# Kernel tuning notes

Measured on AMD Instinct MI355X. Metric: run time of the kernel, lower is better.

Reference implementation:

```python
import jax, jax.numpy as jnp
import numpy as np

D_MODEL = 512
N_HEADS = 8
B, S = 2, 2048


def setup_inputs() -> dict:
    key = jax.random.key(0)
    ks = jax.random.split(key, 7)
    scale = 1.0 / np.sqrt(D_MODEL)
    return {
        "q": jax.random.normal(ks[0], (B, S, D_MODEL), jnp.float32),
        "k": jax.random.normal(ks[1], (B, S, D_MODEL), jnp.float32),
        "v": jax.random.normal(ks[2], (B, S, D_MODEL), jnp.float32),
        "Wq_w": jax.random.normal(ks[3], (D_MODEL, D_MODEL), jnp.float32) * scale,
        "Wq_b": jnp.zeros((D_MODEL,), jnp.float32),
        "Wc_w": jax.random.normal(ks[4], (D_MODEL, D_MODEL), jnp.float32) * scale,
        "Wc_b": jnp.zeros((D_MODEL,), jnp.float32),
    }


def _split(x, n_heads):
    b, s, d = x.shape
    return x.reshape(b, s, n_heads, d // n_heads).transpose(0, 2, 1, 3)  # [b,h,s,dh]


def reference(q, k, v, Wq_w, Wq_b, Wc_w, Wc_b):
    # NOTE: original code (faithfully) projects q, k, v all with W_q.
    qp = q @ Wq_w.T + Wq_b
    kp = k @ Wq_w.T + Wq_b
    vp = v @ Wq_w.T + Wq_b
    qh = _split(qp, N_HEADS)  # [b,h,s,dh]
    kh = _split(kp, N_HEADS)
    vh = _split(vp, N_HEADS)
    d_tensor = qh.shape[-1]
    scores = jnp.einsum("bhqd,bhkd->bhqk", qh, kh) / jnp.sqrt(jnp.float32(d_tensor))
    att = jax.nn.softmax(scores, axis=-1)
    out = jnp.einsum("bhqk,bhkd->bhqd", att, vh)
    b, h, s, dh = out.shape
    out = out.transpose(0, 2, 1, 3).reshape(b, s, h * dh)
    return out @ Wc_w.T + Wc_b
```

## Files before the change

### kernel.cpp

```cpp
#include <hip/hip_runtime.h>
#include <hip/hip_bf16.h>
#include <stdint.h>


typedef __bf16 bf16;
typedef __bf16 bvec8 __attribute__((ext_vector_type(8)));
typedef __bf16 bvec4 __attribute__((ext_vector_type(4)));
typedef float  fvec4 __attribute__((ext_vector_type(4)));
typedef float  fvec16 __attribute__((ext_vector_type(16)));
typedef int    ivec4 __attribute__((ext_vector_type(4)));

#define MFMA16(a, b, c) __builtin_amdgcn_mfma_f32_16x16x32_bf16(a, b, c, 0, 0, 0)
#define MFMA32(a, b, c) __builtin_amdgcn_mfma_f32_32x32x16_bf16(a, b, c, 0, 0, 0)

__device__ __forceinline__ void async16(const void* g, void* l) {
  __builtin_amdgcn_global_load_lds(
      (__attribute__((address_space(1))) void*)(g),
      (__attribute__((address_space(3))) void*)(l), 16, 0, 0);
}

__global__ void cvt_all(const float* __restrict__ q, const float* __restrict__ k,
                        const float* __restrict__ v, const float* __restrict__ Wq,
                        const float* __restrict__ Wc, bf16* __restrict__ qkvb,
                        bf16* __restrict__ Wq16, bf16* __restrict__ Wc16) {
  const int t = blockIdx.x * 256 + threadIdx.x;
  const float* src;
  bf16* dst;
  size_t i;
  if (t < 786432) {
    const int which = t >> 18;
    i = (size_t)(t & 262143);
    src = (which == 0) ? q : (which == 1) ? k : v;
    dst = qkvb + ((size_t)which << 21);
  } else if (t < 819200) {
    src = Wq; dst = Wq16; i = (size_t)(t - 786432);
  } else {
    src = Wc; dst = Wc16; i = (size_t)(t - 819200);
  }
  fvec4 a = *(const fvec4*)(src + i * 8);
  fvec4 b = *(const fvec4*)(src + i * 8 + 4);
  bvec8 o;
#pragma unroll
  for (int j = 0; j < 4; ++j) { o[j] = (bf16)a[j]; o[j + 4] = (bf16)b[j]; }
  *(bvec8*)(dst + i * 8) = o;
}

template <bool PROJ, typename OutT>
__launch_bounds__(256, 3)
__global__ void gemm512(const bf16* __restrict__ X, const bf16* __restrict__ W,
                        const float* __restrict__ bias, OutT* __restrict__ Y,
                        bf16* __restrict__ Yt) {
  __shared__ __attribute__((aligned(16))) char As[2][64 * 128];
  __shared__ __attribute__((aligned(16))) char Bs[2][128 * 128];

  const int tid = threadIdx.x;
  const int w = tid >> 6, l = tid & 63;
  const int wr = w >> 1, wc = w & 1;
  const int l15 = l & 15, lg = l >> 4;
  const int bm0 = blockIdx.x * 64;
  const int bn0 = blockIdx.y * 128;

  fvec4 acc[2][4] = {};

  auto stageA = [&](int buf, int k0) {
#pragma unroll
    for (int j = 0; j < 2; ++j) {
      int c = j * 256 + w * 64 + l;
      int row = c >> 3;
      int g = (c & 7) ^ (row & 7);
      async16(X + (size_t)(bm0 + row) * 512 + k0 + g * 8, &As[buf][c * 16]);
    }
  };
  auto stageB = [&](int buf, int k0) {
#pragma unroll
    for (int j = 0; j < 4; ++j) {
      int c = j * 256 + w * 64 + l;
      int row = c >> 3;
      int g = (c & 7) ^ (row & 7);
      async16(W + (size_t)(bn0 + row) * 512 + k0 + g * 8, &Bs[buf][c * 16]);
    }
  };

  stageA(0, 0);
  stageB(0, 0);
  __syncthreads();

  for (int t = 0; t < 8; ++t) {
    const int buf = t & 1;
    if (t < 7) { stageA(buf ^ 1, (t + 1) * 64); stageB(buf ^ 1, (t + 1) * 64); }
#pragma unroll
    for (int kk = 0; kk < 2; ++kk) {
      bvec8 af[2], bfr[4];
      const int g = kk * 4 + lg;
#pragma unroll
      for (int m = 0; m < 2; ++m) {
        int r = wr * 32 + m * 16 + l15;
        af[m] = *(const bvec8*)&As[buf][r * 128 + ((g ^ (r & 7)) << 4)];
      }
#pragma unroll
      for (int n = 0; n < 4; ++n) {
        int r = wc * 64 + n * 16 + l15;
        bfr[n] = *(const bvec8*)&Bs[buf][r * 128 + ((g ^ (r & 7)) << 4)];
      }
#pragma unroll
      for (int m = 0; m < 2; ++m)
#pragma unroll
        for (int n = 0; n < 4; ++n) acc[m][n] = MFMA16(af[m], bfr[n], acc[m][n]);
    }
    __syncthreads();
  }

  const bool trans = PROJ && (bm0 >= 8192);
#pragma unroll
  for (int n = 0; n < 4; ++n) {
    const int col = bn0 + wc * 64 + n * 16 + l15;
    const float bv = bias[col];
#pragma unroll
    for (int m = 0; m < 2; ++m) {
      const int row0 = bm0 + wr * 32 + m * 16 + lg * 4;
      if (!trans) {
#pragma unroll
        for (int r = 0; r < 4; ++r)
          Y[(size_t)(row0 + r) * 512 + col] = (OutT)(acc[m][n][r] + bv);
      } else {
        const int m0 = row0 - 8192;
        const int b = m0 >> 11, s = m0 & 2047;
        bvec4 v4;
#pragma unroll
        for (int r = 0; r < 4; ++r) v4[r] = (bf16)(acc[m][n][r] + bv);
        *(bvec4*)&Yt[(size_t)(b * 512 + col) * 2048 + s] = v4;
      }
    }
  }
}

__launch_bounds__(256, 3)
__global__ void attn_kernel(const bf16* __restrict__ qp, const bf16* __restrict__ kp,
                            const bf16* __restrict__ vt, bf16* __restrict__ po01,
                            bf16* __restrict__ po23, float* __restrict__ pl) {
  __shared__ __attribute__((aligned(16))) char Ks[2][64 * 128];
  __shared__ __attribute__((aligned(16))) char Vs[2][64 * 128];

  const int tid = threadIdx.x;
  const int w = tid >> 6, l = tid & 63;
  const int l31 = l & 31, hi = l >> 5;
  const int bh = blockIdx.y, b = bh >> 3, h = bh & 7;
  const int half = blockIdx.z;
  const int kvbase = half * 512;
  const int qw0 = blockIdx.x * 128 + w * 32;

  const bf16* kbase = kp + (size_t)(b * 2048) * 512 + h * 64;
  const bf16* vbase = vt + (size_t)(b * 512 + h * 64) * 2048;

  bvec8 qf[4];
  {
    const bf16* qrow = qp + (size_t)(b * 2048 + qw0 + l31) * 512 + h * 64 + hi * 8;
#pragma unroll
    for (int ks = 0; ks < 4; ++ks) qf[ks] = *(const bvec8*)(qrow + ks * 16);
  }

  auto stageK = [&](int buf, int kv0) {
#pragma unroll
    for (int j = 0; j < 2; ++j) {
      int c = j * 256 + tid;
      int row = c >> 3;
      int g = (c & 7) ^ (row & 7);
      async16(kbase + (size_t)(kv0 + row) * 512 + g * 8, &Ks[buf][c * 16]);
    }
  };
  auto stageV = [&](int buf, int kv0) {
#pragma unroll
    for (int j = 0; j < 2; ++j) {
      int c = j * 256 + tid;
      int row = c >> 3;
      int g = (c & 7) ^ (row & 7);
      async16(vbase + (size_t)row * 2048 + kv0 + g * 8, &Vs[buf][c * 16]);
    }
  };

  fvec16 oacc[2] = {};
  float l_run = 0.f;

  stageK(0, kvbase);
  stageV(0, kvbase);
  __syncthreads();

  const float SC = 0.125f * 1.44269504089f;

  for (int t = 0; t < 8; ++t) {
    const int buf = t & 1;
    if (t < 7) {
      stageK(buf ^ 1, kvbase + (t + 1) * 64);
      stageV(buf ^ 1, kvbase + (t + 1) * 64);
    }

    fvec16 sac[2] = {};
    __builtin_amdgcn_s_setprio(1);
#pragma unroll
    for (int ks = 0; ks < 4; ++ks) {
      const int chunk = ks * 2 + hi;
#pragma unroll
      for (int kvb = 0; kvb < 2; ++kvb) {
        const int r = kvb * 32 + l31;
        bvec8 kf = *(const bvec8*)&Ks[buf][r * 128 + ((chunk ^ (r & 7)) << 4)];
        sac[kvb] = MFMA32(kf, qf[ks], sac[kvb]);
      }
    }
    __builtin_amdgcn_s_setprio(0);

    ivec4 pw[4];
    float psum = 0.f;
#pragma unroll
    for (int f = 0; f < 2; ++f) {
      float p[16];
#pragma unroll
      for (int r2 = 0; r2 < 16; ++r2) {
        p[r2] = exp2f(sac[f][r2] * SC);
        psum += p[r2];
      }
      int wv[4][2];
#pragma unroll
      for (int m = 0; m < 4; ++m)
#pragma unroll
        for (int i = 0; i < 2; ++i)
          asm("v_cvt_pk_bf16_f32 %0, %1, %2"
              : "=v"(wv[m][i]) : "v"(p[4 * m + 2 * i]), "v"(p[4 * m + 2 * i + 1]));
#pragma unroll
      for (int i = 0; i < 2; ++i) {
        int a0 = wv[0][i], c0 = wv[1][i];
        asm volatile("v_permlane32_swap_b32 %0, %1" : "+v"(a0), "+v"(c0));
        pw[2 * f][i] = a0; pw[2 * f][2 + i] = c0;
        int a1 = wv[2][i], c1 = wv[3][i];
        asm volatile("v_permlane32_swap_b32 %0, %1" : "+v"(a1), "+v"(c1));
        pw[2 * f + 1][i] = a1; pw[2 * f + 1][2 + i] = c1;
      }
    }
    l_run += psum;

    __builtin_amdgcn_s_setprio(1);
#pragma unroll
    for (int ks = 0; ks < 4; ++ks) {
      const bvec8 pb = __builtin_bit_cast(bvec8, pw[ks]);
      const int chunk = ks * 2 + hi;
#pragma unroll
      for (int dhb = 0; dhb < 2; ++dhb) {
        const int r = dhb * 32 + l31;
        bvec8 vf = *(const bvec8*)&Vs[buf][r * 128 + ((chunk ^ (r & 7)) << 4)];
        oacc[dhb] = MFMA32(pb, vf, oacc[dhb]);
      }
    }
    __builtin_amdgcn_s_setprio(0);
    __syncthreads();
  }

  bf16* pob = ((half < 2) ? po01 : po23) + (size_t)(half & 1) * 2097152;
#pragma unroll
  for (int dhb = 0; dhb < 2; ++dhb)
#pragma unroll
    for (int r2 = 0; r2 < 16; ++r2) {
      const int q = qw0 + (r2 & 3) + 8 * (r2 >> 2) + 4 * hi;
      pob[(size_t)(b * 2048 + q) * 512 + h * 64 + dhb * 32 + l31] =
          (bf16)oacc[dhb][r2];
    }
  l_run += __shfl_xor(l_run, 32);
  if (hi == 0)
    pl[half * 32768 + (b * 2048 + qw0 + l31) * 8 + h] = l_run;
}

__global__ void combine_kernel(const bf16* __restrict__ po01, const bf16* __restrict__ po23,
                               const float* __restrict__ pl, bf16* __restrict__ att) {
  const int t = blockIdx.x * 256 + threadIdx.x;
  const int row = t >> 6;
  const int c8 = (t & 63) << 3;
  const int h = c8 >> 6;
  const float inv = 1.0f / (pl[row * 8 + h] + pl[32768 + row * 8 + h] +
                            pl[65536 + row * 8 + h] + pl[98304 + row * 8 + h]);
  bvec8 a0 = *(const bvec8*)(po01 + (size_t)row * 512 + c8);
  bvec8 a1 = *(const bvec8*)(po01 + 2097152 + (size_t)row * 512 + c8);
  bvec8 a2 = *(const bvec8*)(po23 + (size_t)row * 512 + c8);
  bvec8 a3 = *(const bvec8*)(po23 + 2097152 + (size_t)row * 512 + c8);
  bvec8 o;
#pragma unroll
  for (int j = 0; j < 8; ++j)
    o[j] = (bf16)((((float)a0[j] + (float)a1[j]) + ((float)a2[j] + (float)a3[j])) * inv);
  *(bvec8*)(att + (size_t)row * 512 + c8) = o;
}

extern "C" void kernel_launch(void* const* d_in, const int* in_sizes, int n_in,
                              void* d_out, int out_size, void* d_ws, size_t ws_size,
                              hipStream_t stream) {
  const float* q   = (const float*)d_in[0];
  const float* k   = (const float*)d_in[1];
  const float* v   = (const float*)d_in[2];
  const float* Wq  = (const float*)d_in[3];
  const float* Wqb = (const float*)d_in[4];
  const float* Wc  = (const float*)d_in[5];
  const float* Wcb = (const float*)d_in[6];
  float* out = (float*)d_out;

  char* ws = (char*)d_ws;
  const size_t MB = 1u << 20;
  bf16* qkvb = (bf16*)(ws);
  bf16* po01 = (bf16*)(ws);
  bf16* att  = (bf16*)(ws + 8 * MB);
  bf16* Wq16 = (bf16*)(ws + 12 * MB);
  bf16* Wc16 = (bf16*)(ws + 12 * MB + 512 * 1024);
  bf16* qkp  = (bf16*)(ws + 13 * MB);
  bf16* vt   = (bf16*)(ws + 21 * MB);
  bf16* po23 = (bf16*)(ws + 25 * MB);
  float* pl  = (float*)(ws + 33 * MB);

  dim3 bb(256);
  hipLaunchKernelGGL(cvt_all, dim3(3328), bb, 0, stream, q, k, v, Wq, Wc,
                     qkvb, Wq16, Wc16);
  hipLaunchKernelGGL((gemm512<true, bf16>), dim3(192, 4), bb, 0, stream,
                     qkvb, Wq16, Wqb, qkp, vt);
  hipLaunchKernelGGL(attn_kernel, dim3(16, 16, 4), bb, 0, stream,
                     qkp, qkp + 2097152, vt, po01, po23, pl);
  hipLaunchKernelGGL(combine_kernel, dim3(1024), bb, 0, stream, po01, po23, pl, att);
  hipLaunchKernelGGL((gemm512<false, float>), dim3(64, 4), bb, 0, stream,
                     att, Wc16, Wcb, out, nullptr);
}
```

Before: 69.97 us.

## Fuse fp32-to-bf16 conversion into GEMM loads and drop the convert kernel

```diff
diff --git a/kernel.cpp b/kernel.cpp
--- a/kernel.cpp
+++ b/kernel.cpp
@@ -19,37 +19,13 @@
       (__attribute__((address_space(3))) void*)(l), 16, 0, 0);
 }
 
-__global__ void cvt_all(const float* __restrict__ q, const float* __restrict__ k,
-                        const float* __restrict__ v, const float* __restrict__ Wq,
-                        const float* __restrict__ Wc, bf16* __restrict__ qkvb,
-                        bf16* __restrict__ Wq16, bf16* __restrict__ Wc16) {
-  const int t = blockIdx.x * 256 + threadIdx.x;
-  const float* src;
-  bf16* dst;
-  size_t i;
-  if (t < 786432) {
-    const int which = t >> 18;
-    i = (size_t)(t & 262143);
-    src = (which == 0) ? q : (which == 1) ? k : v;
-    dst = qkvb + ((size_t)which << 21);
-  } else if (t < 819200) {
-    src = Wq; dst = Wq16; i = (size_t)(t - 786432);
-  } else {
-    src = Wc; dst = Wc16; i = (size_t)(t - 819200);
-  }
-  fvec4 a = *(const fvec4*)(src + i * 8);
-  fvec4 b = *(const fvec4*)(src + i * 8 + 4);
-  bvec8 o;
-#pragma unroll
-  for (int j = 0; j < 4; ++j) { o[j] = (bf16)a[j]; o[j + 4] = (bf16)b[j]; }
-  *(bvec8*)(dst + i * 8) = o;
-}
-
 template <bool PROJ, typename OutT>
 __launch_bounds__(256, 3)
-__global__ void gemm512(const bf16* __restrict__ X, const bf16* __restrict__ W,
-                        const float* __restrict__ bias, OutT* __restrict__ Y,
-                        bf16* __restrict__ Yt) {
+__global__ void gemm_f32(const bf16* __restrict__ Abf,
+                         const float* __restrict__ Aq, const float* __restrict__ Ak,
+                         const float* __restrict__ Av, const float* __restrict__ Wf,
+                         const float* __restrict__ bias,
+                         OutT* __restrict__ Y, bf16* __restrict__ Yt) {
   __shared__ __attribute__((aligned(16))) char As[2][64 * 128];
   __shared__ __attribute__((aligned(16))) char Bs[2][128 * 128];
 
@@ -60,34 +36,82 @@
   const int bm0 = blockIdx.x * 64;
   const int bn0 = blockIdx.y * 128;
 
+  const float* Xs = nullptr;
+  int arow0 = 0;
+  if constexpr (PROJ) {
+    Xs = (bm0 < 4096) ? Aq : (bm0 < 8192) ? Ak : Av;
+    arow0 = bm0 & 4095;
+  }
+
   fvec4 acc[2][4] = {};
-
-  auto stageA = [&](int buf, int k0) {
+  fvec4 ra[2][2];
+  fvec4 rb[4][2];
+
+  auto loadA = [&](int k0) {
+    if constexpr (PROJ) {
+#pragma unroll
+      for (int j = 0; j < 2; ++j) {
+        int c = j * 256 + tid;
+        int row = c >> 3, g = (c & 7) ^ (row & 7);
+        const float* p = Xs + (size_t)(arow0 + row) * 512 + k0 + g * 8;
+        ra[j][0] = *(const fvec4*)p;
+        ra[j][1] = *(const fvec4*)(p + 4);
+      }
+    }
+  };
+  auto writeA = [&](int buf) {
+    if constexpr (PROJ) {
+#pragma unroll
+      for (int j = 0; j < 2; ++j) {
+        int c = j * 256 + tid;
+        bvec8 o;
+#pragma unroll
+        for (int e = 0; e < 4; ++e) { o[e] = (bf16)ra[j][0][e]; o[4 + e] = (bf16)ra[j][1][e]; }
+        *(bvec8*)&As[buf][c * 16] = o;
+      }
+    }
+  };
+  auto dmaA = [&](int buf, int k0) {
 #pragma unroll
     for (int j = 0; j < 2; ++j) {
-      int c = j * 256 + w * 64 + l;
-      int row = c >> 3;
-      int g = (c & 7) ^ (row & 7);
-      async16(X + (size_t)(bm0 + row) * 512 + k0 + g * 8, &As[buf][c * 16]);
-    }
-  };
-  auto stageB = [&](int buf, int k0) {
+      int c = j * 256 + tid;
+      int row = c >> 3, g = (c & 7) ^ (row & 7);
+      async16(Abf + (size_t)(bm0 + row) * 512 + k0 + g * 8, &As[buf][c * 16]);
+    }
+  };
+  auto loadB = [&](int k0) {
 #pragma unroll
     for (int j = 0; j < 4; ++j) {
-      int c = j * 256 + w * 64 + l;
-      int row = c >> 3;
-      int g = (c & 7) ^ (row & 7);
-      async16(W + (size_t)(bn0 + row) * 512 + k0 + g * 8, &Bs[buf][c * 16]);
-    }
-  };
-
-  stageA(0, 0);
-  stageB(0, 0);
+      int c = j * 256 + tid;
+      int row = c >> 3, g = (c & 7) ^ (row & 7);
+      const float* p = Wf + (size_t)(bn0 + row) * 512 + k0 + g * 8;
+      rb[j][0] = *(const fvec4*)p;
+      rb[j][1] = *(const fvec4*)(p + 4);
+    }
+  };
+  auto writeB = [&](int buf) {
+#pragma unroll
+    for (int j = 0; j < 4; ++j) {
+      int c = j * 256 + tid;
+      bvec8 o;
+#pragma unroll
+      for (int e = 0; e < 4; ++e) { o[e] = (bf16)rb[j][0][e]; o[4 + e] = (bf16)rb[j][1][e]; }
+      *(bvec8*)&Bs[buf][c * 16] = o;
+    }
+  };
+
+  if constexpr (PROJ) loadA(0); else dmaA(0, 0);
+  loadB(0);
+  writeA(0);
+  writeB(0);
   __syncthreads();
 
   for (int t = 0; t < 8; ++t) {
     const int buf = t & 1;
-    if (t < 7) { stageA(buf ^ 1, (t + 1) * 64); stageB(buf ^ 1, (t + 1) * 64); }
+    if (t < 7) {
+      if constexpr (PROJ) loadA((t + 1) * 64); else dmaA(buf ^ 1, (t + 1) * 64);
+      loadB((t + 1) * 64);
+    }
 #pragma unroll
     for (int kk = 0; kk < 2; ++kk) {
       bvec8 af[2], bfr[4];
@@ -106,6 +130,10 @@
       for (int m = 0; m < 2; ++m)
 #pragma unroll
         for (int n = 0; n < 4; ++n) acc[m][n] = MFMA16(af[m], bfr[n], acc[m][n]);
+    }
+    if (t < 7) {
+      writeA(buf ^ 1);
+      writeB(buf ^ 1);
     }
     __syncthreads();
   }
@@ -134,7 +162,7 @@
   }
 }
 
-__launch_bounds__(256, 3)
+__launch_bounds__(256, 4)
 __global__ void attn_kernel(const bf16* __restrict__ qp, const bf16* __restrict__ kp,
                             const bf16* __restrict__ vt, bf16* __restrict__ po01,
                             bf16* __restrict__ po23, float* __restrict__ pl) {
@@ -163,8 +191,7 @@
 #pragma unroll
     for (int j = 0; j < 2; ++j) {
       int c = j * 256 + tid;
-      int row = c >> 3;
-      int g = (c & 7) ^ (row & 7);
+      int row = c >> 3, g = (c & 7) ^ (row & 7);
       async16(kbase + (size_t)(kv0 + row) * 512 + g * 8, &Ks[buf][c * 16]);
     }
   };
@@ -172,8 +199,7 @@
 #pragma unroll
     for (int j = 0; j < 2; ++j) {
       int c = j * 256 + tid;
-      int row = c >> 3;
-      int g = (c & 7) ^ (row & 7);
+      int row = c >> 3, g = (c & 7) ^ (row & 7);
       async16(vbase + (size_t)row * 2048 + kv0 + g * 8, &Vs[buf][c * 16]);
     }
   };
@@ -300,24 +326,21 @@
 
   char* ws = (char*)d_ws;
   const size_t MB = 1u << 20;
-  bf16* qkvb = (bf16*)(ws);
   bf16* po01 = (bf16*)(ws);
   bf16* att  = (bf16*)(ws + 8 * MB);
-  bf16* Wq16 = (bf16*)(ws + 12 * MB);
-  bf16* Wc16 = (bf16*)(ws + 12 * MB + 512 * 1024);
   bf16* qkp  = (bf16*)(ws + 13 * MB);
   bf16* vt   = (bf16*)(ws + 21 * MB);
   bf16* po23 = (bf16*)(ws + 25 * MB);
   float* pl  = (float*)(ws + 33 * MB);
 
   dim3 bb(256);
-  hipLaunchKernelGGL(cvt_all, dim3(3328), bb, 0, stream, q, k, v, Wq, Wc,
-                     qkvb, Wq16, Wc16);
-  hipLaunchKernelGGL((gemm512<true, bf16>), dim3(192, 4), bb, 0, stream,
-                     qkvb, Wq16, Wqb, qkp, vt);
+  hipLaunchKernelGGL((gemm_f32<true, bf16>), dim3(192, 4), bb, 0, stream,
+                     (const bf16*)nullptr, q, k, v, Wq, Wqb, qkp, vt);
   hipLaunchKernelGGL(attn_kernel, dim3(16, 16, 4), bb, 0, stream,
                      qkp, qkp + 2097152, vt, po01, po23, pl);
-  hipLaunchKernelGGL(combine_kernel, dim3(1024), bb, 0, stream, po01, po23, pl, att);
-  hipLaunchKernelGGL((gemm512<false, float>), dim3(64, 4), bb, 0, stream,
-                     att, Wc16, Wcb, out, nullptr);
-}
+  hipLaunchKernelGGL(combine_kernel, dim3(1024), bb, 0, stream,
+                     po01, po23, pl, att);
+  hipLaunchKernelGGL((gemm_f32<false, float>), dim3(64, 4), bb, 0, stream,
+                     att, (const float*)nullptr, (const float*)nullptr,
+                     (const float*)nullptr, Wc, Wcb, out, (bf16*)nullptr);
+}
```

Measured after the change: 72.10 us. 1.03x slower.

## Fuse split-KV combine into output projection GEMM and remap attention blocks

Applied to the files above, without the earlier changes.

```diff
diff --git a/kernel.cpp b/kernel.cpp
--- a/kernel.cpp
+++ b/kernel.cpp
@@ -45,11 +45,10 @@
   *(bvec8*)(dst + i * 8) = o;
 }
 
-template <bool PROJ, typename OutT>
 __launch_bounds__(256, 3)
-__global__ void gemm512(const bf16* __restrict__ X, const bf16* __restrict__ W,
-                        const float* __restrict__ bias, OutT* __restrict__ Y,
-                        bf16* __restrict__ Yt) {
+__global__ void proj_gemm(const bf16* __restrict__ X, const bf16* __restrict__ W,
+                          const float* __restrict__ bias, bf16* __restrict__ Y,
+                          bf16* __restrict__ Yt) {
   __shared__ __attribute__((aligned(16))) char As[2][64 * 128];
   __shared__ __attribute__((aligned(16))) char Bs[2][128 * 128];
 
@@ -65,18 +64,16 @@
   auto stageA = [&](int buf, int k0) {
 #pragma unroll
     for (int j = 0; j < 2; ++j) {
-      int c = j * 256 + w * 64 + l;
-      int row = c >> 3;
-      int g = (c & 7) ^ (row & 7);
+      int c = j * 256 + tid;
+      int row = c >> 3, g = (c & 7) ^ (row & 7);
       async16(X + (size_t)(bm0 + row) * 512 + k0 + g * 8, &As[buf][c * 16]);
     }
   };
   auto stageB = [&](int buf, int k0) {
 #pragma unroll
     for (int j = 0; j < 4; ++j) {
-      int c = j * 256 + w * 64 + l;
-      int row = c >> 3;
-      int g = (c & 7) ^ (row & 7);
+      int c = j * 256 + tid;
+      int row = c >> 3, g = (c & 7) ^ (row & 7);
       async16(W + (size_t)(bn0 + row) * 512 + k0 + g * 8, &Bs[buf][c * 16]);
     }
   };
@@ -110,7 +107,7 @@
     __syncthreads();
   }
 
-  const bool trans = PROJ && (bm0 >= 8192);
+  const bool trans = (bm0 >= 8192);
 #pragma unroll
   for (int n = 0; n < 4; ++n) {
     const int col = bn0 + wc * 64 + n * 16 + l15;
@@ -121,7 +118,7 @@
       if (!trans) {
 #pragma unroll
         for (int r = 0; r < 4; ++r)
-          Y[(size_t)(row0 + r) * 512 + col] = (OutT)(acc[m][n][r] + bv);
+          Y[(size_t)(row0 + r) * 512 + col] = (bf16)(acc[m][n][r] + bv);
       } else {
         const int m0 = row0 - 8192;
         const int b = m0 >> 11, s = m0 & 2047;
@@ -134,7 +131,7 @@
   }
 }
 
-__launch_bounds__(256, 3)
+__launch_bounds__(256, 4)
 __global__ void attn_kernel(const bf16* __restrict__ qp, const bf16* __restrict__ kp,
                             const bf16* __restrict__ vt, bf16* __restrict__ po01,
                             bf16* __restrict__ po23, float* __restrict__ pl) {
@@ -144,10 +141,13 @@
   const int tid = threadIdx.x;
   const int w = tid >> 6, l = tid & 63;
   const int l31 = l & 31, hi = l >> 5;
-  const int bh = blockIdx.y, b = bh >> 3, h = bh & 7;
-  const int half = blockIdx.z;
+
+  const int lin = blockIdx.x;
+  const int work = (lin & 7) * 128 + (lin >> 3);
+  const int qb = work & 15, bh = (work >> 4) & 15, half = work >> 8;
+  const int b = bh >> 3, h = bh & 7;
   const int kvbase = half * 512;
-  const int qw0 = blockIdx.x * 128 + w * 32;
+  const int qw0 = qb * 128 + w * 32;
 
   const bf16* kbase = kp + (size_t)(b * 2048) * 512 + h * 64;
   const bf16* vbase = vt + (size_t)(b * 512 + h * 64) * 2048;
@@ -163,8 +163,7 @@
 #pragma unroll
     for (int j = 0; j < 2; ++j) {
       int c = j * 256 + tid;
-      int row = c >> 3;
-      int g = (c & 7) ^ (row & 7);
+      int row = c >> 3, g = (c & 7) ^ (row & 7);
       async16(kbase + (size_t)(kv0 + row) * 512 + g * 8, &Ks[buf][c * 16]);
     }
   };
@@ -172,8 +171,7 @@
 #pragma unroll
     for (int j = 0; j < 2; ++j) {
       int c = j * 256 + tid;
-      int row = c >> 3;
-      int g = (c & 7) ^ (row & 7);
+      int row = c >> 3, g = (c & 7) ^ (row & 7);
       async16(vbase + (size_t)row * 2048 + kv0 + g * 8, &Vs[buf][c * 16]);
     }
   };
@@ -267,23 +265,107 @@
     pl[half * 32768 + (b * 2048 + qw0 + l31) * 8 + h] = l_run;
 }
 
-__global__ void combine_kernel(const bf16* __restrict__ po01, const bf16* __restrict__ po23,
-                               const float* __restrict__ pl, bf16* __restrict__ att) {
-  const int t = blockIdx.x * 256 + threadIdx.x;
-  const int row = t >> 6;
-  const int c8 = (t & 63) << 3;
-  const int h = c8 >> 6;
-  const float inv = 1.0f / (pl[row * 8 + h] + pl[32768 + row * 8 + h] +
-                            pl[65536 + row * 8 + h] + pl[98304 + row * 8 + h]);
-  bvec8 a0 = *(const bvec8*)(po01 + (size_t)row * 512 + c8);
-  bvec8 a1 = *(const bvec8*)(po01 + 2097152 + (size_t)row * 512 + c8);
-  bvec8 a2 = *(const bvec8*)(po23 + (size_t)row * 512 + c8);
-  bvec8 a3 = *(const bvec8*)(po23 + 2097152 + (size_t)row * 512 + c8);
-  bvec8 o;
-#pragma unroll
-  for (int j = 0; j < 8; ++j)
-    o[j] = (bf16)((((float)a0[j] + (float)a1[j]) + ((float)a2[j] + (float)a3[j])) * inv);
-  *(bvec8*)(att + (size_t)row * 512 + c8) = o;
+__launch_bounds__(256, 3)
+__global__ void out_gemm(const bf16* __restrict__ po01, const bf16* __restrict__ po23,
+                         const float* __restrict__ pl, const bf16* __restrict__ W,
+                         const float* __restrict__ bias, float* __restrict__ Y) {
+  __shared__ __attribute__((aligned(16))) char As[2][64 * 128];
+  __shared__ __attribute__((aligned(16))) char Bs[2][128 * 128];
+
+  const int tid = threadIdx.x;
+  const int w = tid >> 6, l = tid & 63;
+  const int wr = w >> 1, wc = w & 1;
+  const int l15 = l & 15, lg = l >> 4;
+  const int bm0 = blockIdx.x * 64;
+  const int bn0 = blockIdx.y * 128;
+
+  fvec4 acc[2][4] = {};
+
+  bvec8 rp[2][4];
+  fvec4 rl[2];
+
+  auto loadA = [&](int k0) {
+#pragma unroll
+    for (int j = 0; j < 2; ++j) {
+      int c = j * 256 + tid;
+      int row = c >> 3, g = (c & 7) ^ (row & 7);
+      const size_t off = (size_t)(bm0 + row) * 512 + k0 + g * 8;
+      rp[j][0] = *(const bvec8*)(po01 + off);
+      rp[j][1] = *(const bvec8*)(po01 + 2097152 + off);
+      rp[j][2] = *(const bvec8*)(po23 + off);
+      rp[j][3] = *(const bvec8*)(po23 + 2097152 + off);
+      const int ridx = (bm0 + row) * 8 + ((k0 + g * 8) >> 6);
+      rl[j] = fvec4{pl[ridx], pl[32768 + ridx], pl[65536 + ridx], pl[98304 + ridx]};
+    }
+  };
+  auto writeA = [&](int buf) {
+#pragma unroll
+    for (int j = 0; j < 2; ++j) {
+      int c = j * 256 + tid;
+      const float inv = 1.0f / (rl[j][0] + rl[j][1] + rl[j][2] + rl[j][3]);
+      bvec8 o;
+#pragma unroll
+      for (int e = 0; e < 8; ++e)
+        o[e] = (bf16)((((float)rp[j][0][e] + (float)rp[j][1][e]) +
+                       ((float)rp[j][2][e] + (float)rp[j][3][e])) * inv);
+      *(bvec8*)&As[buf][c * 16] = o;
+    }
+  };
+  auto stageB = [&](int buf, int k0) {
+#pragma unroll
+    for (int j = 0; j < 4; ++j) {
+      int c = j * 256 + tid;
+      int row = c >> 3, g = (c & 7) ^ (row & 7);
+      async16(W + (size_t)(bn0 + row) * 512 + k0 + g * 8, &Bs[buf][c * 16]);
+    }
+  };
+
+  loadA(0);
+  stageB(0, 0);
+  writeA(0);
+  __syncthreads();
+
+  for (int t = 0; t < 8; ++t) {
+    const int buf = t & 1;
+    if (t < 7) {
+      loadA((t + 1) * 64);
+      stageB(buf ^ 1, (t + 1) * 64);
+    }
+#pragma unroll
+    for (int kk = 0; kk < 2; ++kk) {
+      bvec8 af[2], bfr[4];
+      const int g = kk * 4 + lg;
+#pragma unroll
+      for (int m = 0; m < 2; ++m) {
+        int r = wr * 32 + m * 16 + l15;
+        af[m] = *(const bvec8*)&As[buf][r * 128 + ((g ^ (r & 7)) << 4)];
+      }
+#pragma unroll
+      for (int n = 0; n < 4; ++n) {
+        int r = wc * 64 + n * 16 + l15;
+        bfr[n] = *(const bvec8*)&Bs[buf][r * 128 + ((g ^ (r & 7)) << 4)];
+      }
+#pragma unroll
+      for (int m = 0; m < 2; ++m)
+#pragma unroll
+        for (int n = 0; n < 4; ++n) acc[m][n] = MFMA16(af[m], bfr[n], acc[m][n]);
+    }
+    if (t < 7) writeA(buf ^ 1);
+    __syncthreads();
+  }
+
+#pragma unroll
+  for (int n = 0; n < 4; ++n) {
+    const int col = bn0 + wc * 64 + n * 16 + l15;
+    const float bv = bias[col];
+#pragma unroll
+    for (int m = 0; m < 2; ++m) {
+      const int row0 = bm0 + wr * 32 + m * 16 + lg * 4;
+#pragma unroll
+      for (int r = 0; r < 4; ++r)
+        Y[(size_t)(row0 + r) * 512 + col] = acc[m][n][r] + bv;
+    }
+  }
 }
 
 extern "C" void kernel_launch(void* const* d_in, const int* in_sizes, int n_in,
@@ -302,7 +384,6 @@
   const size_t MB = 1u << 20;
   bf16* qkvb = (bf16*)(ws);
   bf16* po01 = (bf16*)(ws);
-  bf16* att  = (bf16*)(ws + 8 * MB);
   bf16* Wq16 = (bf16*)(ws + 12 * MB);
   bf16* Wc16 = (bf16*)(ws + 12 * MB + 512 * 1024);
   bf16* qkp  = (bf16*)(ws + 13 * MB);
@@ -313,11 +394,10 @@
   dim3 bb(256);
   hipLaunchKernelGGL(cvt_all, dim3(3328), bb, 0, stream, q, k, v, Wq, Wc,
                      qkvb, Wq16, Wc16);
-  hipLaunchKernelGGL((gemm512<true, bf16>), dim3(192, 4), bb, 0, stream,
+  hipLaunchKernelGGL(proj_gemm, dim3(192, 4), bb, 0, stream,
                      qkvb, Wq16, Wqb, qkp, vt);
-  hipLaunchKernelGGL(attn_kernel, dim3(16, 16, 4), bb, 0, stream,
+  hipLaunchKernelGGL(attn_kernel, dim3(1024), bb, 0, stream,
                      qkp, qkp + 2097152, vt, po01, po23, pl);
-  hipLaunchKernelGGL(combine_kernel, dim3(1024), bb, 0, stream, po01, po23, pl, att);
-  hipLaunchKernelGGL((gemm512<false, float>), dim3(64, 4), bb, 0, stream,
-                     att, Wc16, Wcb, out, nullptr);
-}
+  hipLaunchKernelGGL(out_gemm, dim3(64, 4), bb, 0, stream,
+                     po01, po23, pl, Wc16, Wcb, out);
+}
```

Result: slower. 72.36 us (+3.4%).
